# Performance work log

Measured on AMD Instinct MI355X. Metric: run time of the kernel, lower is better.

Reference implementation:

```python
import jax, jax.numpy as jnp
import numpy as np

BSZ, K, N_DIM, N_DATA = 16, 65536, 128, 1000000
T, M = 0.07, 0.5


def setup_inputs() -> dict:
    key = jax.random.key(0)
    k1, k2, k3, k4, k5 = jax.random.split(key, 5)
    x = jax.random.normal(k1, (BSZ, N_DIM), dtype=jnp.float32)
    z = jax.random.normal(k2, (BSZ, N_DIM), dtype=jnp.float32)
    y = jax.random.randint(k3, (BSZ,), 0, N_DATA)
    idx = jax.random.randint(k4, (BSZ, K), 0, N_DATA)
    mem = jax.random.normal(k5, (N_DATA, N_DIM), dtype=jnp.float32)
    mem = mem / jnp.linalg.norm(mem, axis=1, keepdims=True)  # F.normalize at init
    return {"x": x, "z": z, "memory": mem, "y": y, "idx": idx}


def reference(x, z, memory, y, idx):
    n_data = memory.shape[0]
    # gather positive row + K negative rows per sample -> [bsz, K+1, n_dim]
    m_pos = memory[y]                 # [bsz, n_dim]
    w_neg = memory[idx]               # [bsz, K, n_dim]
    W = jnp.concatenate([m_pos[:, None, :], w_neg], axis=1)
    # batched dot products (bmm with x.unsqueeze(2)) then temperature scale
    lx = jnp.einsum('bkd,bd->bk', W, x) / T
    lz = jnp.einsum('bkd,bd->bk', W, z) / T
    # use_softmax=False branch: exp then divide by normalization constant Z_0
    lx = jnp.exp(lx)
    lz = jnp.exp(lz)
    # first call: z0 < 0, so Z_0 is set to lx.mean() * n_data (detached scalar)
    z0 = jax.lax.stop_gradient(lx.mean() * n_data)
    lx = lx / z0
    lz = lz / z0
    # EMA memory update (no-grad): w_pos = m*mem[y] + (1-m)*x, renormalize, scatter
    w_pos = m_pos * M + x * (1.0 - M)
    w_pos = w_pos / jnp.linalg.norm(w_pos, axis=1, keepdims=True)
    new_memory = memory.at[y].set(w_pos)
    return lx, lz, new_memory
```

## Files before the change

### kernel.cpp

```cpp
#include <hip/hip_runtime.h>
#include <math.h>

#define BSZ   16
#define NDIM  128
#define KNEG  65536
#define KP1   65537
#define NDATA 1000000
#define NROWS (BSZ * KP1)
#define NPART 1024
#define INV_T (1.0f / 0.07f)

__global__ __launch_bounds__(256) void gather_dot_kernel(
    const float* __restrict__ mem, const float* __restrict__ x,
    const float* __restrict__ z, const int* __restrict__ y,
    const int* __restrict__ idx, float* __restrict__ out_lx,
    float* __restrict__ out_lz, double* __restrict__ partials)
{
    __shared__ float s_lx[8];
    const int tid   = threadIdx.x;
    const int group = tid >> 5;
    const int lane  = tid & 31;
    const int r     = blockIdx.x * 8 + group;

    const int b = r / KP1;
    const int k = r - b * KP1;
    const int row = (k == 0) ? y[b] : idx[b * KNEG + (k - 1)];

    const float4* mrow = (const float4*)(mem + (size_t)row * NDIM);
    const float4* xr   = (const float4*)(x + b * NDIM);
    const float4* zr   = (const float4*)(z + b * NDIM);

    float4 mv = mrow[lane];
    float4 xv = xr[lane];
    float4 zv = zr[lane];

    float px = mv.x * xv.x + mv.y * xv.y + mv.z * xv.z + mv.w * xv.w;
    float pz = mv.x * zv.x + mv.y * zv.y + mv.z * zv.z + mv.w * zv.w;

    #pragma unroll
    for (int m = 16; m >= 1; m >>= 1) {
        px += __shfl_xor(px, m, 64);
        pz += __shfl_xor(pz, m, 64);
    }

    if (lane == 0) {
        float lxv = expf(px * INV_T);
        float lzv = expf(pz * INV_T);
        out_lx[r] = lxv;
        out_lz[r] = lzv;
        s_lx[group] = lxv;
    }
    __syncthreads();
    if (tid == 0) {
        double s = 0.0;
        #pragma unroll
        for (int g = 0; g < 8; ++g) s += (double)s_lx[g];
        atomicAdd(&partials[blockIdx.x & (NPART - 1)], s);
    }
}

__global__ void finalize_kernel(double* __restrict__ ws)
{
    __shared__ double sh[256];
    double s = 0.0;
    for (int i = threadIdx.x; i < NPART; i += 256) s += ws[i];
    sh[threadIdx.x] = s;
    __syncthreads();
    for (int off = 128; off >= 1; off >>= 1) {
        if (threadIdx.x < off) sh[threadIdx.x] += sh[threadIdx.x + off];
        __syncthreads();
    }
    if (threadIdx.x == 0) {
        double z0 = (sh[0] / (double)NROWS) * (double)NDATA;
        ws[NPART] = 1.0 / z0;
    }
}

__global__ __launch_bounds__(256) void copy_mem_kernel(
    const float4* __restrict__ src, float4* __restrict__ dst)
{
    const int n4 = NDATA * NDIM / 4;
    const int stride = gridDim.x * blockDim.x;
    for (int i = blockIdx.x * blockDim.x + threadIdx.x; i < n4; i += stride)
        dst[i] = src[i];
}

__global__ __launch_bounds__(256) void scale_kernel(
    float4* __restrict__ lxlz, const double* __restrict__ ws)
{
    const float s = (float)ws[NPART];
    const int n4 = 2 * NROWS / 4;
    const int stride = gridDim.x * blockDim.x;
    for (int i = blockIdx.x * blockDim.x + threadIdx.x; i < n4; i += stride) {
        float4 v = lxlz[i];
        v.x *= s; v.y *= s; v.z *= s; v.w *= s;
        lxlz[i] = v;
    }
}

__global__ void update_rows_kernel(
    const float* __restrict__ mem, const float* __restrict__ x,
    const int* __restrict__ y, float* __restrict__ out_mem)
{
    const int lane = threadIdx.x;
    for (int b = 0; b < BSZ; ++b) {
        const int row = y[b];
        const size_t mo = (size_t)row * NDIM;
        float2 m  = ((const float2*)(mem + mo))[lane];
        float2 xv = ((const float2*)(x + (size_t)b * NDIM))[lane];
        float w0 = 0.5f * m.x + 0.5f * xv.x;
        float w1 = 0.5f * m.y + 0.5f * xv.y;
        float ss = w0 * w0 + w1 * w1;
        #pragma unroll
        for (int mk = 32; mk >= 1; mk >>= 1) ss += __shfl_xor(ss, mk, 64);
        float inv = 1.0f / sqrtf(ss);
        ((float2*)(out_mem + mo))[lane] = make_float2(w0 * inv, w1 * inv);
    }
}

extern "C" void kernel_launch(void* const* d_in, const int* in_sizes, int n_in,
                              void* d_out, int out_size, void* d_ws, size_t ws_size,
                              hipStream_t stream)
{
    const float* x   = (const float*)d_in[0];
    const float* z   = (const float*)d_in[1];
    const float* mem = (const float*)d_in[2];
    const int*   y   = (const int*)d_in[3];
    const int*   idx = (const int*)d_in[4];

    float* out_lx  = (float*)d_out;
    float* out_lz  = out_lx + NROWS;
    float* out_mem = out_lz + NROWS;
    double* ws     = (double*)d_ws;

    hipMemsetAsync(d_ws, 0, NPART * sizeof(double), stream);

    gather_dot_kernel<<<NROWS / 8, 256, 0, stream>>>(
        mem, x, z, y, idx, out_lx, out_lz, ws);
    finalize_kernel<<<1, 256, 0, stream>>>(ws);
    copy_mem_kernel<<<8192, 256, 0, stream>>>(
        (const float4*)mem, (float4*)out_mem);
    scale_kernel<<<2048, 256, 0, stream>>>((float4*)d_out, ws);
    update_rows_kernel<<<1, 64, 0, stream>>>(mem, x, y, out_mem);
}
```

Baseline: 990.9 us.

## Fuse memory copy into gather kernel and merge finalize, scale, update kernels

The full memory copy is folded into the gather-dot kernel, with each thread copying one float4 alongside its gather work. This overlaps the streaming copy with the latency-bound random row gathers. The finalize, scale and row-update kernels merge into a single kernel. Each scale block recomputes the reduction of partials, and separate blocks perform the EMA row updates with a last-writer check for duplicate indices. This removes several launches and serial single-block stages, at the cost of higher per-block register use and redundant reductions.

```diff
diff --git a/kernel.cpp b/kernel.cpp
--- a/kernel.cpp
+++ b/kernel.cpp
@@ -10,29 +10,38 @@
 #define NPART 1024
 #define INV_T (1.0f / 0.07f)
 
-__global__ __launch_bounds__(256) void gather_dot_kernel(
+#define GBLK  (NROWS / 8)
+#define N4MEM (NDATA * (NDIM / 4))
+#define SCALE_BLK 2048
+#define N4LX  (2 * NROWS / 4)
+
+__global__ __launch_bounds__(256) void fused_main_kernel(
     const float* __restrict__ mem, const float* __restrict__ x,
     const float* __restrict__ z, const int* __restrict__ y,
     const int* __restrict__ idx, float* __restrict__ out_lx,
-    float* __restrict__ out_lz, double* __restrict__ partials)
+    float* __restrict__ out_lz, float* __restrict__ out_mem,
+    double* __restrict__ partials)
 {
     __shared__ float s_lx[8];
-    const int tid   = threadIdx.x;
+    const int tid = threadIdx.x;
+    const int bid = blockIdx.x;
+
+    const size_t ci = (size_t)bid * 256 + tid;
+    const bool do_copy = (ci < (size_t)N4MEM);
+    float4 cv;
+    if (do_copy) cv = ((const float4*)mem)[ci];
+
     const int group = tid >> 5;
     const int lane  = tid & 31;
-    const int r     = blockIdx.x * 8 + group;
+    const int r     = bid * 8 + group;
 
-    const int b = r / KP1;
-    const int k = r - b * KP1;
+    const int b   = r / KP1;
+    const int k   = r - b * KP1;
     const int row = (k == 0) ? y[b] : idx[b * KNEG + (k - 1)];
 
-    const float4* mrow = (const float4*)(mem + (size_t)row * NDIM);
-    const float4* xr   = (const float4*)(x + b * NDIM);
-    const float4* zr   = (const float4*)(z + b * NDIM);
-
-    float4 mv = mrow[lane];
-    float4 xv = xr[lane];
-    float4 zv = zr[lane];
+    float4 mv = ((const float4*)(mem + (size_t)row * NDIM))[lane];
+    float4 xv = ((const float4*)(x + b * NDIM))[lane];
+    float4 zv = ((const float4*)(z + b * NDIM))[lane];
 
     float px = mv.x * xv.x + mv.y * xv.y + mv.z * xv.z + mv.w * xv.w;
     float pz = mv.x * zv.x + mv.y * zv.y + mv.z * zv.z + mv.w * zv.w;
@@ -50,71 +59,63 @@
         out_lz[r] = lzv;
         s_lx[group] = lxv;
     }
+
+    if (do_copy) ((float4*)out_mem)[ci] = cv;
+
     __syncthreads();
     if (tid == 0) {
         double s = 0.0;
         #pragma unroll
         for (int g = 0; g < 8; ++g) s += (double)s_lx[g];
-        atomicAdd(&partials[blockIdx.x & (NPART - 1)], s);
+        atomicAdd(&partials[bid & (NPART - 1)], s);
     }
 }
 
-__global__ void finalize_kernel(double* __restrict__ ws)
+__global__ __launch_bounds__(256) void finish_kernel(
+    const float* __restrict__ mem, const float* __restrict__ x,
+    const int* __restrict__ y, const double* __restrict__ partials,
+    float4* __restrict__ lxlz, float* __restrict__ out_mem)
 {
-    __shared__ double sh[256];
-    double s = 0.0;
-    for (int i = threadIdx.x; i < NPART; i += 256) s += ws[i];
-    sh[threadIdx.x] = s;
-    __syncthreads();
-    for (int off = 128; off >= 1; off >>= 1) {
-        if (threadIdx.x < off) sh[threadIdx.x] += sh[threadIdx.x + off];
+    const int tid = threadIdx.x;
+    const int bid = blockIdx.x;
+
+    if (bid < SCALE_BLK) {
+        __shared__ double sh[256];
+        double s = 0.0;
+        #pragma unroll
+        for (int i = 0; i < NPART / 256; ++i) s += partials[tid + i * 256];
+        sh[tid] = s;
         __syncthreads();
-    }
-    if (threadIdx.x == 0) {
-        double z0 = (sh[0] / (double)NROWS) * (double)NDATA;
-        ws[NPART] = 1.0 / z0;
-    }
-}
-
-__global__ __launch_bounds__(256) void copy_mem_kernel(
-    const float4* __restrict__ src, float4* __restrict__ dst)
-{
-    const int n4 = NDATA * NDIM / 4;
-    const int stride = gridDim.x * blockDim.x;
-    for (int i = blockIdx.x * blockDim.x + threadIdx.x; i < n4; i += stride)
-        dst[i] = src[i];
-}
-
-__global__ __launch_bounds__(256) void scale_kernel(
-    float4* __restrict__ lxlz, const double* __restrict__ ws)
-{
-    const float s = (float)ws[NPART];
-    const int n4 = 2 * NROWS / 4;
-    const int stride = gridDim.x * blockDim.x;
-    for (int i = blockIdx.x * blockDim.x + threadIdx.x; i < n4; i += stride) {
-        float4 v = lxlz[i];
-        v.x *= s; v.y *= s; v.z *= s; v.w *= s;
-        lxlz[i] = v;
-    }
-}
-
-__global__ void update_rows_kernel(
-    const float* __restrict__ mem, const float* __restrict__ x,
-    const int* __restrict__ y, float* __restrict__ out_mem)
-{
-    const int lane = threadIdx.x;
-    for (int b = 0; b < BSZ; ++b) {
+        #pragma unroll
+        for (int off = 128; off >= 1; off >>= 1) {
+            if (tid < off) sh[tid] += sh[tid + off];
+            __syncthreads();
+        }
+        const double z0 = (sh[0] / (double)NROWS) * (double)NDATA;
+        const float  sc = (float)(1.0 / z0);
+        for (int i = bid * 256 + tid; i < N4LX; i += SCALE_BLK * 256) {
+            float4 v = lxlz[i];
+            v.x *= sc; v.y *= sc; v.z *= sc; v.w *= sc;
+            lxlz[i] = v;
+        }
+    } else {
+        const int b   = bid - SCALE_BLK;
         const int row = y[b];
-        const size_t mo = (size_t)row * NDIM;
-        float2 m  = ((const float2*)(mem + mo))[lane];
-        float2 xv = ((const float2*)(x + (size_t)b * NDIM))[lane];
-        float w0 = 0.5f * m.x + 0.5f * xv.x;
-        float w1 = 0.5f * m.y + 0.5f * xv.y;
-        float ss = w0 * w0 + w1 * w1;
-        #pragma unroll
-        for (int mk = 32; mk >= 1; mk >>= 1) ss += __shfl_xor(ss, mk, 64);
-        float inv = 1.0f / sqrtf(ss);
-        ((float2*)(out_mem + mo))[lane] = make_float2(w0 * inv, w1 * inv);
+        bool last = true;
+        for (int j = b + 1; j < BSZ; ++j)
+            if (y[j] == row) last = false;
+        if (last && tid < 64) {
+            float2 m  = ((const float2*)(mem + (size_t)row * NDIM))[tid];
+            float2 xv = ((const float2*)(x + (size_t)b * NDIM))[tid];
+            float w0 = 0.5f * m.x + 0.5f * xv.x;
+            float w1 = 0.5f * m.y + 0.5f * xv.y;
+            float ss = w0 * w0 + w1 * w1;
+            #pragma unroll
+            for (int mk = 32; mk >= 1; mk >>= 1) ss += __shfl_xor(ss, mk, 64);
+            const float inv = 1.0f / sqrtf(ss);
+            ((float2*)(out_mem + (size_t)row * NDIM))[tid] =
+                make_float2(w0 * inv, w1 * inv);
+        }
     }
 }
 
@@ -135,11 +136,9 @@
 
     hipMemsetAsync(d_ws, 0, NPART * sizeof(double), stream);
 
-    gather_dot_kernel<<<NROWS / 8, 256, 0, stream>>>(
-        mem, x, z, y, idx, out_lx, out_lz, ws);
-    finalize_kernel<<<1, 256, 0, stream>>>(ws);
-    copy_mem_kernel<<<8192, 256, 0, stream>>>(
-        (const float4*)mem, (float4*)out_mem);
-    scale_kernel<<<2048, 256, 0, stream>>>((float4*)d_out, ws);
-    update_rows_kernel<<<1, 64, 0, stream>>>(mem, x, y, out_mem);
+    fused_main_kernel<<<GBLK, 256, 0, stream>>>(
+        mem, x, z, y, idx, out_lx, out_lz, out_mem, ws);
+
+    finish_kernel<<<SCALE_BLK + BSZ, 256, 0, stream>>>(
+        mem, x, y, ws, (float4*)d_out, out_mem);
 }
```

Result: faster. 894.5 us (-9.7%).
